# Optimization experiments

Measured on AMD Instinct MI355X. Metric: run time of the kernel, lower is better.

Reference implementation:

```python
import jax, jax.numpy as jnp
import numpy as np

N = 50000      # nodes
E = 800000     # edges per relation/layer
L = 2          # GCN layer_num
D = 128        # input_dim == output_dim


def setup_inputs() -> dict:
    key = jax.random.key(0)
    ks = jax.random.split(key, 11)
    x = jax.random.normal(ks[0], (N, D), jnp.float32)
    hidden = jax.random.normal(ks[1], (N, D), jnp.float32)
    adj_src = jax.random.randint(ks[2], (L, E), 0, N)
    adj_dst = jax.random.randint(ks[3], (L, E), 0, N)
    adj_w = jax.random.uniform(ks[4], (L, E), jnp.float32)
    std = 1.0 / np.sqrt(D)  # reset_parameters: uniform(-std, std)
    def u(k, shape):
        return jax.random.uniform(k, shape, jnp.float32, -std, std)
    gcn_W = u(ks[5], (L, D, D))
    gcn_b = u(ks[6], (L, D))
    x2h_W = u(ks[7], (D, 3 * D))
    x2h_b = u(ks[8], (3 * D,))
    h2h_W = u(ks[9], (D, 3 * D))
    h2h_b = u(ks[10], (3 * D,))
    return dict(x=x, hidden=hidden, adj_src=adj_src, adj_dst=adj_dst, adj_w=adj_w,
                gcn_W=gcn_W, gcn_b=gcn_b, x2h_W=x2h_W, x2h_b=x2h_b,
                h2h_W=h2h_W, h2h_b=h2h_b)


def reference(x, hidden, adj_src, adj_dst, adj_w, gcn_W, gcn_b,
              x2h_W, x2h_b, h2h_W, h2h_b):
    # MRGCN: layer_num GCN layers, layer l uses relation l's sparse adjacency.
    h = x
    for l in range(L):
        support = h @ gcn_W[l]                              # [N, D]
        msg = support[adj_src[l]] * adj_w[l][:, None]       # [E, D] irregular gather
        agg = jax.ops.segment_sum(msg, adj_dst[l], num_segments=N)  # spmm scatter-add
        h = jax.nn.relu(agg + gcn_b[l])
    # GRU gate chain (dropout=0 / eval mode)
    gate_x = h @ x2h_W + x2h_b                              # [N, 3D]
    gate_h = hidden @ h2h_W + h2h_b                         # [N, 3D]
    i_r, i_i, i_n = jnp.split(gate_x, 3, axis=1)
    h_r, h_i, h_n = jnp.split(gate_h, 3, axis=1)
    resetgate = jax.nn.sigmoid(i_r + h_r)
    inputgate = jax.nn.sigmoid(i_i + h_i)
    newgate = jnp.tanh(i_n + resetgate * h_n)
    hy = newgate + inputgate * (hidden - newgate)
    return hy
```

## Files before the change

kernel.cpp:

```cpp
#include <hip/hip_runtime.h>

#define D 128
#define RPW 8
#define ROWS_PB 32

typedef __attribute__((ext_vector_type(8))) short short8;
typedef __attribute__((ext_vector_type(4))) float f32x4;

static __device__ __forceinline__ ushort f2bf(float f) {
    unsigned u = __float_as_uint(f);
    unsigned r = (u + 0x7fffu + ((u >> 16) & 1u)) >> 16;
    return (ushort)r;
}

static __device__ __forceinline__ void gemm_body(float* sw, float (*sh)[D],
                                                 const float* __restrict__ in,
                                                 const float* __restrict__ W,
                                                 ushort* __restrict__ outb,
                                                 int N, int bid, int tid) {
    int row0 = bid * ROWS_PB;
    for (int j = tid; j < D * D / 4; j += 256)
        ((float4*)sw)[j] = ((const float4*)W)[j];
    for (int i = tid; i < ROWS_PB * (D / 4); i += 256) {
        int r = i >> 5, c4 = i & 31;
        int row = row0 + r;
        float4 v = (row < N) ? ((const float4*)(in + (size_t)row * D))[c4]
                             : make_float4(0.f, 0.f, 0.f, 0.f);
        ((float4*)sh)[i] = v;
    }
    __syncthreads();
    int wid = tid >> 6, lane = tid & 63;
    int rb = wid * RPW;
    float acc0[RPW], acc1[RPW];
#pragma unroll
    for (int r = 0; r < RPW; ++r) { acc0[r] = 0.f; acc1[r] = 0.f; }
    for (int k = 0; k < D; k += 4) {
        float w0[4], w1[4];
#pragma unroll
        for (int kk = 0; kk < 4; ++kk) {
            w0[kk] = sw[(k + kk) * D + lane];
            w1[kk] = sw[(k + kk) * D + lane + 64];
        }
#pragma unroll
        for (int r = 0; r < RPW; ++r) {
            float4 a4 = *(const float4*)&sh[rb + r][k];
            acc0[r] = fmaf(a4.x, w0[0], acc0[r]); acc1[r] = fmaf(a4.x, w1[0], acc1[r]);
            acc0[r] = fmaf(a4.y, w0[1], acc0[r]); acc1[r] = fmaf(a4.y, w1[1], acc1[r]);
            acc0[r] = fmaf(a4.z, w0[2], acc0[r]); acc1[r] = fmaf(a4.z, w1[2], acc1[r]);
            acc0[r] = fmaf(a4.w, w0[3], acc0[r]); acc1[r] = fmaf(a4.w, w1[3], acc1[r]);
        }
    }
#pragma unroll
    for (int r = 0; r < RPW; ++r) {
        int row = row0 + rb + r;
        if (row < N) {
            outb[(size_t)row * D + lane] = f2bf(acc0[r]);
            outb[(size_t)row * D + lane + 64] = f2bf(acc1[r]);
        }
    }
}

__global__ __launch_bounds__(256) void fused_sgc(const float* __restrict__ x,
                                                 const float* __restrict__ W0,
                                                 ushort* __restrict__ Abf, int N,
                                                 const int* __restrict__ adj_dst,
                                                 int* __restrict__ counts,
                                                 ushort* __restrict__ pl, int E2, int E,
                                                 const float* __restrict__ Wx,
                                                 const float* __restrict__ Wh,
                                                 ushort* __restrict__ wxt,
                                                 ushort* __restrict__ wht,
                                                 int GB, int SB) {
    __shared__ float sw[D * D];
    __shared__ float sh[ROWS_PB][D];
    int bid = blockIdx.x, tid = threadIdx.x;
    if (bid < GB) {
        gemm_body(sw, sh, x, W0, Abf, N, bid, tid);
    } else if (bid < GB + SB) {
        int i = (bid - GB) * 256 + tid;
        if (i < E2) {
            int off = (i >= E) ? N : 0;
            pl[i] = (ushort)atomicAdd(&counts[off + adj_dst[i]], 1);
        }
    } else {
        int i = (bid - GB - SB) * 256 + tid;
        if (i < 384 * 128) {
            int c = i >> 7, k = i & 127;
            wxt[i] = f2bf(Wx[(size_t)k * 384 + c]);
            wht[i] = f2bf(Wh[(size_t)k * 384 + c]);
        }
    }
}

__global__ __launch_bounds__(256) void gemm_rowbatch_bf(const float* __restrict__ in,
                                                        const float* __restrict__ W,
                                                        ushort* __restrict__ outb, int N) {
    __shared__ float sw[D * D];
    __shared__ float sh[ROWS_PB][D];
    gemm_body(sw, sh, in, W, outb, N, blockIdx.x, threadIdx.x);
}

__global__ void zero_int4(int4* __restrict__ p, int n4) {
    int i = blockIdx.x * blockDim.x + threadIdx.x;
    if (i < n4) p[i] = make_int4(0, 0, 0, 0);
}

__global__ __launch_bounds__(256) void scan_partial(const int4* __restrict__ counts4,
                                                    int* __restrict__ bsum) {
    int b = blockIdx.x, t = threadIdx.x;
    int4 c0 = counts4[(size_t)b * 512 + t * 2];
    int4 c1 = counts4[(size_t)b * 512 + t * 2 + 1];
    int s = c0.x + c0.y + c0.z + c0.w + c1.x + c1.y + c1.z + c1.w;
#pragma unroll
    for (int d = 1; d < 64; d <<= 1) s += __shfl_xor(s, d);
    __shared__ int ws[4];
    if ((t & 63) == 0) ws[t >> 6] = s;
    __syncthreads();
    if (t == 0) bsum[b] = ws[0] + ws[1] + ws[2] + ws[3];
}

__global__ void scan_base(const int* __restrict__ bsum, int* __restrict__ bbase, int nb) {
    int lane = threadIdx.x;
    int run = 0;
    for (int c = 0; c < nb; c += 64) {
        int v = (c + lane < nb) ? bsum[c + lane] : 0;
        int inc = v;
#pragma unroll
        for (int d = 1; d < 64; d <<= 1) {
            int y = __shfl_up(inc, d);
            if (lane >= d) inc += y;
        }
        if (c + lane < nb) bbase[c + lane] = run + inc - v;
        run += __shfl(inc, 63);
    }
}

__global__ __launch_bounds__(256) void scan_apply(const int4* __restrict__ counts4,
                                                  const int* __restrict__ bbase,
                                                  int4* __restrict__ off4) {
    __shared__ int ts[256];
    int b = blockIdx.x, t = threadIdx.x;
    int4 c0 = counts4[(size_t)b * 512 + t * 2];
    int4 c1 = counts4[(size_t)b * 512 + t * 2 + 1];
    int s = c0.x + c0.y + c0.z + c0.w + c1.x + c1.y + c1.z + c1.w;
    ts[t] = s;
    __syncthreads();
    for (int d = 1; d < 256; d <<= 1) {
        int x = ts[t];
        int y = (t >= d) ? ts[t - d] : 0;
        __syncthreads();
        ts[t] = x + y;
        __syncthreads();
    }
    int base = bbase[b] + ((t == 0) ? 0 : ts[t - 1]);
    int4 o0, o1;
    o0.x = base;
    o0.y = o0.x + c0.x;
    o0.z = o0.y + c0.y;
    o0.w = o0.z + c0.z;
    o1.x = o0.w + c0.w;
    o1.y = o1.x + c1.x;
    o1.z = o1.y + c1.y;
    o1.w = o1.z + c1.z;
    off4[(size_t)b * 512 + t * 2] = o0;
    off4[(size_t)b * 512 + t * 2 + 1] = o1;
}

__global__ void place2_kernel(const int* __restrict__ src, const int* __restrict__ dst,
                              const float* __restrict__ w,
                              const int* __restrict__ offsets2,
                              const ushort* __restrict__ pl,
                              int2* __restrict__ srcw0, int2* __restrict__ srcw1,
                              int E, int E2, int N) {
    int i = blockIdx.x * blockDim.x + threadIdx.x;
    if (i >= E2) return;
    int l1 = i >= E;
    int node = dst[i];
    int p = offsets2[(l1 ? N : 0) + node] - (l1 ? E : 0) + (int)pl[i];
    int2 v = make_int2(src[i], __float_as_int(w[i]));
    (l1 ? srcw1 : srcw0)[p] = v;
}

__global__ void gather_nodes(const ushort* __restrict__ supb, const int2* __restrict__ srcw,
                             const int* __restrict__ offsets, int sub,
                             const float* __restrict__ bias,
                             float* __restrict__ out, int N) {
    int node = (blockIdx.x * blockDim.x + threadIdx.x) >> 6;
    int lane = threadIdx.x & 63;
    if (node >= N) return;
    int lo = offsets[node] - sub, hi = offsets[node + 1] - sub;
    float ax = 0.f, ay = 0.f;
    int c = lane * 2;
    const ushort* base = supb + c;
    int j = lo;
    for (; j + 8 <= hi; j += 8) {
        int2 s[8];
        uint v[8];
#pragma unroll
        for (int u = 0; u < 8; ++u) s[u] = srcw[j + u];
#pragma unroll
        for (int u = 0; u < 8; ++u)
            v[u] = *(const uint*)(base + ((size_t)s[u].x << 7));
#pragma unroll
        for (int u = 0; u < 8; ++u) {
            float wt = __int_as_float(s[u].y);
            ax = fmaf(wt, __uint_as_float(v[u] << 16), ax);
            ay = fmaf(wt, __uint_as_float(v[u] & 0xffff0000u), ay);
        }
    }
    for (; j < hi; ++j) {
        int2 sw = srcw[j];
        float wt = __int_as_float(sw.y);
        uint v = *(const uint*)(base + ((size_t)sw.x << 7));
        ax = fmaf(wt, __uint_as_float(v << 16), ax);
        ay = fmaf(wt, __uint_as_float(v & 0xffff0000u), ay);
    }
    float2 bi = *(const float2*)(bias + c);
    float2 o;
    o.x = fmaxf(ax + bi.x, 0.f);
    o.y = fmaxf(ay + bi.y, 0.f);
    *(float2*)(out + (size_t)node * D + c) = o;
}

#define QROWS 192
#define KPAD 136
__global__ __launch_bounds__(256) void gru_mfma_lds(const float* __restrict__ h,
                                                    const float* __restrict__ hidden,
                                                    const ushort* __restrict__ wxt,
                                                    const ushort* __restrict__ wht,
                                                    const float* __restrict__ bx,
                                                    const float* __restrict__ bh,
                                                    float* __restrict__ out, int N) {
    __shared__ ushort lw[QROWS * KPAD];
    int tid = threadIdx.x;
    int wid = tid >> 6, lane = tid & 63;
    int nstripes = (N + 15) >> 4;
    int stripe = blockIdx.x * 4 + wid;
    bool live = stripe < nstripes;
    int row0 = stripe * 16;
    int lr = lane & 15;
    int lk = (lane >> 4) * 8;

    short8 Ah[4], Ad[4];
    if (live) {
        const float* hrow = h + (size_t)(row0 + lr) * D + lk;
        const float* drow = hidden + (size_t)(row0 + lr) * D + lk;
#pragma unroll
        for (int ks = 0; ks < 4; ++ks) {
            float4 a0 = *(const float4*)(hrow + ks * 32);
            float4 a1 = *(const float4*)(hrow + ks * 32 + 4);
            float4 c0 = *(const float4*)(drow + ks * 32);
            float4 c1 = *(const float4*)(drow + ks * 32 + 4);
            short8 va, vc;
            va[0] = f2bf(a0.x); va[1] = f2bf(a0.y); va[2] = f2bf(a0.z); va[3] = f2bf(a0.w);
            va[4] = f2bf(a1.x); va[5] = f2bf(a1.y); va[6] = f2bf(a1.z); va[7] = f2bf(a1.w);
            vc[0] = f2bf(c0.x); vc[1] = f2bf(c0.y); vc[2] = f2bf(c0.z); vc[3] = f2bf(c0.w);
            vc[4] = f2bf(c1.x); vc[5] = f2bf(c1.y); vc[6] = f2bf(c1.z); vc[7] = f2bf(c1.w);
            Ah[ks] = va;
            Ad[ks] = vc;
        }
    }
    int orow = row0 + (lane >> 4) * 4;

    for (int q = 0; q < 4; ++q) {
        if (q) __syncthreads();
        for (int j = tid; j < QROWS * 16; j += 256) {
            int chunk = j & 15;
            int row = j >> 4;
            int mat = row >= 96;
            int r = row - (mat ? 96 : 0);
            int g = r >> 5;
            int c = r & 31;
            const ushort* srcp = (mat ? wht : wxt)
                               + ((size_t)(g * 128 + q * 32 + c) << 7) + (chunk << 3);
            *(short8*)&lw[row * KPAD + chunk * 8] = *(const short8*)srcp;
        }
        __syncthreads();
        if (!live) continue;

#pragma unroll
        for (int mt = 0; mt < 2; ++mt) {
            int cl = mt * 16 + lr;
            const ushort* bx0 = lw + (0 * 32 + cl) * KPAD + lk;
            const ushort* bx1 = lw + (1 * 32 + cl) * KPAD + lk;
            const ushort* bx2 = lw + (2 * 32 + cl) * KPAD + lk;
            const ushort* bh0 = lw + ((96 + 0 * 32) + cl) * KPAD + lk;
            const ushort* bh1 = lw + ((96 + 1 * 32) + cl) * KPAD + lk;
            const ushort* bh2 = lw + ((96 + 2 * 32) + cl) * KPAD + lk;
            f32x4 ax0{}, ax1{}, ax2{}, ah0{}, ah1{}, ah2{};
#pragma unroll
            for (int ks = 0; ks < 4; ++ks) {
                short8 w0 = *(const short8*)(bx0 + ks * 32);
                short8 w1 = *(const short8*)(bx1 + ks * 32);
                short8 w2 = *(const short8*)(bx2 + ks * 32);
                short8 v0 = *(const short8*)(bh0 + ks * 32);
                short8 v1 = *(const short8*)(bh1 + ks * 32);
                short8 v2 = *(const short8*)(bh2 + ks * 32);
                ax0 = __builtin_amdgcn_mfma_f32_16x16x32_bf16(Ah[ks], w0, ax0, 0, 0, 0);
                ax1 = __builtin_amdgcn_mfma_f32_16x16x32_bf16(Ah[ks], w1, ax1, 0, 0, 0);
                ax2 = __builtin_amdgcn_mfma_f32_16x16x32_bf16(Ah[ks], w2, ax2, 0, 0, 0);
                ah0 = __builtin_amdgcn_mfma_f32_16x16x32_bf16(Ad[ks], v0, ah0, 0, 0, 0);
                ah1 = __builtin_amdgcn_mfma_f32_16x16x32_bf16(Ad[ks], v1, ah1, 0, 0, 0);
                ah2 = __builtin_amdgcn_mfma_f32_16x16x32_bf16(Ad[ks], v2, ah2, 0, 0, 0);
            }
            int col = q * 32 + mt * 16 + lr;
            float bxr = bx[col], bxi = bx[col + 128], bxn = bx[col + 256];
            float bhr = bh[col], bhi = bh[col + 128], bhn = bh[col + 256];
#pragma unroll
            for (int r = 0; r < 4; ++r) {
                int row = orow + r;
                if (row < N) {
                    float ir = ax0[r] + bxr, hr = ah0[r] + bhr;
                    float ii = ax1[r] + bxi, hi = ah1[r] + bhi;
                    float in_ = ax2[r] + bxn, hn = ah2[r] + bhn;
                    float rg = 1.f / (1.f + __expf(-(ir + hr)));
                    float ig = 1.f / (1.f + __expf(-(ii + hi)));
                    float nx = in_ + rg * hn;
                    float ng = 1.f - 2.f / (__expf(2.f * nx) + 1.f);
                    float hv = hidden[(size_t)row * D + col];
                    out[(size_t)row * D + col] = ng + ig * (hv - ng);
                }
            }
        }
    }
}

extern "C" void kernel_launch(void* const* d_in, const int* in_sizes, int n_in,
                              void* d_out, int out_size, void* d_ws, size_t ws_size,
                              hipStream_t stream) {
    const float* x      = (const float*)d_in[0];
    const float* hidden = (const float*)d_in[1];
    const int*   adj_src = (const int*)d_in[2];
    const int*   adj_dst = (const int*)d_in[3];
    const float* adj_w   = (const float*)d_in[4];
    const float* gcn_W   = (const float*)d_in[5];
    const float* gcn_b   = (const float*)d_in[6];
    const float* x2h_W   = (const float*)d_in[7];
    const float* x2h_b   = (const float*)d_in[8];
    const float* h2h_W   = (const float*)d_in[9];
    const float* h2h_b   = (const float*)d_in[10];
    float* out = (float*)d_out;

    const int L = 2;
    const int N = in_sizes[0] / D;
    const int E = in_sizes[2] / L;
    const size_t nd = (size_t)N * D;

    const int twoN   = 2 * N;
    const int NB     = (twoN + 2047) / 2048;
    const int padded = NB * 2048;

    char* ws = (char*)d_ws;
    ushort* Abf     = (ushort*)ws;                ws += nd * 2;
    float*  B       = (float*)ws;                 ws += nd * 4;
    int*   counts2  = (int*)ws;                   ws += (size_t)padded * 4;
    int*   offsets2 = (int*)ws;                   ws += ((size_t)padded + 64) * 4;
    int*   bsum     = (int*)ws;                   ws += ((size_t)NB + 64) * 4;
    int*   bbase    = (int*)ws;                   ws += ((size_t)NB + 64) * 4;
    int2*  srcw0    = (int2*)ws;                  ws += (size_t)E * 8;
    int2*  srcw1    = (int2*)ws;                  ws += (size_t)E * 8;
    ushort* pl      = (ushort*)ws;                ws += (size_t)2 * E * 2;
    ushort* wxt     = (ushort*)ws;                ws += (size_t)384 * 128 * 2;
    ushort* wht     = (ushort*)ws;                ws += (size_t)384 * 128 * 2;

    dim3 blk(256);
    int batch_blocks = (N + ROWS_PB - 1) / ROWS_PB;
    int gat_blocks   = (N + 3) / 4;
    int e2_blocks    = (2 * E + 255) / 256;
    int zero_blocks  = (padded / 4 + 255) / 256;
    int convw_blocks = (384 * 128 + 255) / 256;
    int nstripes     = (N + 15) / 16;
    int gru_blocks   = (nstripes + 3) / 4;

    zero_int4<<<zero_blocks, blk, 0, stream>>>((int4*)counts2, padded / 4);
    fused_sgc<<<batch_blocks + e2_blocks + convw_blocks, blk, 0, stream>>>(
        x, gcn_W, Abf, N, adj_dst, counts2, pl, 2 * E, E,
        x2h_W, h2h_W, wxt, wht, batch_blocks, e2_blocks);
    scan_partial<<<NB, blk, 0, stream>>>((const int4*)counts2, bsum);
    scan_base<<<1, 64, 0, stream>>>(bsum, bbase, NB);
    scan_apply<<<NB, blk, 0, stream>>>((const int4*)counts2, bbase, (int4*)offsets2);
    place2_kernel<<<e2_blocks, blk, 0, stream>>>(adj_src, adj_dst, adj_w, offsets2, pl,
                                                 srcw0, srcw1, E, 2 * E, N);
    gather_nodes<<<gat_blocks, blk, 0, stream>>>(Abf, srcw0, offsets2, 0,
                                                 gcn_b, B, N);
    gemm_rowbatch_bf<<<batch_blocks, blk, 0, stream>>>(B, gcn_W + (size_t)D * D, Abf, N);
    gather_nodes<<<gat_blocks, blk, 0, stream>>>(Abf, srcw1, offsets2 + N, E,
                                                 gcn_b + D, B, N);
    gru_mfma_lds<<<gru_blocks, blk, 0, stream>>>(B, hidden, wxt, wht, x2h_b, h2h_b, out, N);
}
```

Baseline: 327.3 us.

## Fuse layer-0 gather with layer-1 GEMM and store intermediates in bf16

Layer 0's gather/aggregate is fused with the layer-1 dense GEMM in one kernel. Each wave gathers a row, applies bias and ReLU, then multiplies it by W1 held in LDS, which removes the fp32 intermediate round trip and a kernel launch. The second gather now writes bf16 output, which the GRU kernel loads directly without converting. The first fused kernel also interleaves GEMM blocks with count-atomic blocks in a 1:4 pattern. The fused kernel loads the full 64KB W1 into LDS for every 16-node block, which adds LDS traffic and lowers occupancy, and the per-row GEMM runs serially inside each wave.

```diff
diff --git a/kernel.cpp b/kernel.cpp
--- a/kernel.cpp
+++ b/kernel.cpp
@@ -65,39 +65,35 @@
                                                  ushort* __restrict__ Abf, int N,
                                                  const int* __restrict__ adj_dst,
                                                  int* __restrict__ counts,
-                                                 ushort* __restrict__ pl, int E2, int E,
+                                                 ushort* __restrict__ pl, int E2,
+                                                 int E, int GB,
                                                  const float* __restrict__ Wx,
                                                  const float* __restrict__ Wh,
                                                  ushort* __restrict__ wxt,
-                                                 ushort* __restrict__ wht,
-                                                 int GB, int SB) {
+                                                 ushort* __restrict__ wht) {
     __shared__ float sw[D * D];
     __shared__ float sh[ROWS_PB][D];
     int bid = blockIdx.x, tid = threadIdx.x;
-    if (bid < GB) {
-        gemm_body(sw, sh, x, W0, Abf, N, bid, tid);
-    } else if (bid < GB + SB) {
-        int i = (bid - GB) * 256 + tid;
-        if (i < E2) {
-            int off = (i >= E) ? N : 0;
-            pl[i] = (ushort)atomicAdd(&counts[off + adj_dst[i]], 1);
+    int five = GB * 5;
+    if (bid < five) {
+        int g = bid / 5, j = bid - g * 5;
+        if (j == 0) {
+            gemm_body(sw, sh, x, W0, Abf, N, g, tid);
+        } else {
+            int i = (g * 4 + j - 1) * 256 + tid;
+            if (i < E2) {
+                int off = (i >= E) ? N : 0;
+                pl[i] = (ushort)atomicAdd(&counts[off + adj_dst[i]], 1);
+            }
         }
     } else {
-        int i = (bid - GB - SB) * 256 + tid;
+        int i = (bid - five) * 256 + tid;
         if (i < 384 * 128) {
             int c = i >> 7, k = i & 127;
             wxt[i] = f2bf(Wx[(size_t)k * 384 + c]);
             wht[i] = f2bf(Wh[(size_t)k * 384 + c]);
         }
     }
-}
-
-__global__ __launch_bounds__(256) void gemm_rowbatch_bf(const float* __restrict__ in,
-                                                        const float* __restrict__ W,
-                                                        ushort* __restrict__ outb, int N) {
-    __shared__ float sw[D * D];
-    __shared__ float sh[ROWS_PB][D];
-    gemm_body(sw, sh, in, W, outb, N, blockIdx.x, threadIdx.x);
 }
 
 __global__ void zero_int4(int4* __restrict__ p, int n4) {
@@ -181,17 +177,11 @@
     (l1 ? srcw1 : srcw0)[p] = v;
 }
 
-__global__ void gather_nodes(const ushort* __restrict__ supb, const int2* __restrict__ srcw,
-                             const int* __restrict__ offsets, int sub,
-                             const float* __restrict__ bias,
-                             float* __restrict__ out, int N) {
-    int node = (blockIdx.x * blockDim.x + threadIdx.x) >> 6;
-    int lane = threadIdx.x & 63;
-    if (node >= N) return;
-    int lo = offsets[node] - sub, hi = offsets[node + 1] - sub;
-    float ax = 0.f, ay = 0.f;
-    int c = lane * 2;
-    const ushort* base = supb + c;
+static __device__ __forceinline__ void gather_row(const ushort* __restrict__ base,
+                                                  const int2* __restrict__ srcw,
+                                                  int lo, int hi,
+                                                  float& ax, float& ay) {
+    ax = 0.f; ay = 0.f;
     int j = lo;
     for (; j + 8 <= hi; j += 8) {
         int2 s[8];
@@ -215,16 +205,70 @@
         ax = fmaf(wt, __uint_as_float(v << 16), ax);
         ay = fmaf(wt, __uint_as_float(v & 0xffff0000u), ay);
     }
+}
+
+__global__ __launch_bounds__(256) void gather_gemm(const ushort* __restrict__ supb,
+                                                   const int2* __restrict__ srcw,
+                                                   const int* __restrict__ offsets,
+                                                   const float* __restrict__ bias,
+                                                   const float* __restrict__ W1,
+                                                   ushort* __restrict__ outb, int N) {
+    __shared__ float sw1[D * D];
+    __shared__ float rowbuf[4][D];
+    int tid = threadIdx.x;
+    for (int j = tid; j < D * D / 4; j += 256)
+        ((float4*)sw1)[j] = ((const float4*)W1)[j];
+    __syncthreads();
+    int wid = tid >> 6, lane = tid & 63;
+    int c = lane * 2;
+    const ushort* base = supb + c;
+#pragma unroll
+    for (int r = 0; r < 4; ++r) {
+        int node = blockIdx.x * 16 + wid * 4 + r;
+        if (node >= N) break;
+        int lo = offsets[node], hi = offsets[node + 1];
+        float ax, ay;
+        gather_row(base, srcw, lo, hi, ax, ay);
+        float2 bi = *(const float2*)(bias + c);
+        rowbuf[wid][c] = fmaxf(ax + bi.x, 0.f);
+        rowbuf[wid][c + 1] = fmaxf(ay + bi.y, 0.f);
+        float acc0 = 0.f, acc1 = 0.f;
+        for (int k = 0; k < D; k += 4) {
+            float4 rv = *(const float4*)&rowbuf[wid][k];
+            acc0 = fmaf(rv.x, sw1[(k + 0) * D + lane], acc0);
+            acc1 = fmaf(rv.x, sw1[(k + 0) * D + lane + 64], acc1);
+            acc0 = fmaf(rv.y, sw1[(k + 1) * D + lane], acc0);
+            acc1 = fmaf(rv.y, sw1[(k + 1) * D + lane + 64], acc1);
+            acc0 = fmaf(rv.z, sw1[(k + 2) * D + lane], acc0);
+            acc1 = fmaf(rv.z, sw1[(k + 2) * D + lane + 64], acc1);
+            acc0 = fmaf(rv.w, sw1[(k + 3) * D + lane], acc0);
+            acc1 = fmaf(rv.w, sw1[(k + 3) * D + lane + 64], acc1);
+        }
+        outb[(size_t)node * D + lane] = f2bf(acc0);
+        outb[(size_t)node * D + lane + 64] = f2bf(acc1);
+    }
+}
+
+__global__ void gather_nodes_bf(const ushort* __restrict__ supb,
+                                const int2* __restrict__ srcw,
+                                const int* __restrict__ offsets, int sub,
+                                const float* __restrict__ bias,
+                                ushort* __restrict__ outb, int N) {
+    int node = (blockIdx.x * blockDim.x + threadIdx.x) >> 6;
+    int lane = threadIdx.x & 63;
+    if (node >= N) return;
+    int lo = offsets[node] - sub, hi = offsets[node + 1] - sub;
+    int c = lane * 2;
+    float ax, ay;
+    gather_row(supb + c, srcw, lo, hi, ax, ay);
     float2 bi = *(const float2*)(bias + c);
-    float2 o;
-    o.x = fmaxf(ax + bi.x, 0.f);
-    o.y = fmaxf(ay + bi.y, 0.f);
-    *(float2*)(out + (size_t)node * D + c) = o;
+    uint pk = ((uint)f2bf(fmaxf(ay + bi.y, 0.f)) << 16) | (uint)f2bf(fmaxf(ax + bi.x, 0.f));
+    *(uint*)(outb + (size_t)node * D + c) = pk;
 }
 
 #define QROWS 192
 #define KPAD 136
-__global__ __launch_bounds__(256) void gru_mfma_lds(const float* __restrict__ h,
+__global__ __launch_bounds__(256) void gru_mfma_lds(const ushort* __restrict__ hb,
                                                     const float* __restrict__ hidden,
                                                     const ushort* __restrict__ wxt,
                                                     const ushort* __restrict__ wht,
@@ -243,20 +287,16 @@
 
     short8 Ah[4], Ad[4];
     if (live) {
-        const float* hrow = h + (size_t)(row0 + lr) * D + lk;
+        const ushort* hrow = hb + (size_t)(row0 + lr) * D + lk;
         const float* drow = hidden + (size_t)(row0 + lr) * D + lk;
 #pragma unroll
         for (int ks = 0; ks < 4; ++ks) {
-            float4 a0 = *(const float4*)(hrow + ks * 32);
-            float4 a1 = *(const float4*)(hrow + ks * 32 + 4);
+            Ah[ks] = *(const short8*)(hrow + ks * 32);
             float4 c0 = *(const float4*)(drow + ks * 32);
             float4 c1 = *(const float4*)(drow + ks * 32 + 4);
-            short8 va, vc;
-            va[0] = f2bf(a0.x); va[1] = f2bf(a0.y); va[2] = f2bf(a0.z); va[3] = f2bf(a0.w);
-            va[4] = f2bf(a1.x); va[5] = f2bf(a1.y); va[6] = f2bf(a1.z); va[7] = f2bf(a1.w);
+            short8 vc;
             vc[0] = f2bf(c0.x); vc[1] = f2bf(c0.y); vc[2] = f2bf(c0.z); vc[3] = f2bf(c0.w);
             vc[4] = f2bf(c1.x); vc[5] = f2bf(c1.y); vc[6] = f2bf(c1.z); vc[7] = f2bf(c1.w);
-            Ah[ks] = va;
             Ad[ks] = vc;
         }
     }
@@ -352,7 +392,8 @@
 
     char* ws = (char*)d_ws;
     ushort* Abf     = (ushort*)ws;                ws += nd * 2;
-    float*  B       = (float*)ws;                 ws += nd * 4;
+    ushort* Abf2    = (ushort*)ws;                ws += nd * 2;
+    ushort* Bbf     = (ushort*)ws;                ws += nd * 2;
     int*   counts2  = (int*)ws;                   ws += (size_t)padded * 4;
     int*   offsets2 = (int*)ws;                   ws += ((size_t)padded + 64) * 4;
     int*   bsum     = (int*)ws;                   ws += ((size_t)NB + 64) * 4;
@@ -369,22 +410,23 @@
     int e2_blocks    = (2 * E + 255) / 256;
     int zero_blocks  = (padded / 4 + 255) / 256;
     int convw_blocks = (384 * 128 + 255) / 256;
+    int gg_blocks    = (N + 15) / 16;
     int nstripes     = (N + 15) / 16;
     int gru_blocks   = (nstripes + 3) / 4;
 
     zero_int4<<<zero_blocks, blk, 0, stream>>>((int4*)counts2, padded / 4);
-    fused_sgc<<<batch_blocks + e2_blocks + convw_blocks, blk, 0, stream>>>(
-        x, gcn_W, Abf, N, adj_dst, counts2, pl, 2 * E, E,
-        x2h_W, h2h_W, wxt, wht, batch_blocks, e2_blocks);
+    fused_sgc<<<batch_blocks * 5 + convw_blocks, blk, 0, stream>>>(
+        x, gcn_W, Abf, N, adj_dst, counts2, pl, 2 * E, E, batch_blocks,
+        x2h_W, h2h_W, wxt, wht);
     scan_partial<<<NB, blk, 0, stream>>>((const int4*)counts2, bsum);
     scan_base<<<1, 64, 0, stream>>>(bsum, bbase, NB);
     scan_apply<<<NB, blk, 0, stream>>>((const int4*)counts2, bbase, (int4*)offsets2);
     place2_kernel<<<e2_blocks, blk, 0, stream>>>(adj_src, adj_dst, adj_w, offsets2, pl,
                                                  srcw0, srcw1, E, 2 * E, N);
-    gather_nodes<<<gat_blocks, blk, 0, stream>>>(Abf, srcw0, offsets2, 0,
-                                                 gcn_b, B, N);
-    gemm_rowbatch_bf<<<batch_blocks, blk, 0, stream>>>(B, gcn_W + (size_t)D * D, Abf, N);
-    gather_nodes<<<gat_blocks, blk, 0, stream>>>(Abf, srcw1, offsets2 + N, E,
-                                                 gcn_b + D, B, N);
-    gru_mfma_lds<<<gru_blocks, blk, 0, stream>>>(B, hidden, wxt, wht, x2h_b, h2h_b, out, N);
-}
+    gather_gemm<<<gg_blocks, blk, 0, stream>>>(Abf, srcw0, offsets2, gcn_b,
+                                               gcn_W + (size_t)D * D, Abf2, N);
+    gather_nodes_bf<<<gat_blocks, blk, 0, stream>>>(Abf2, srcw1, offsets2 + N, E,
+                                                    gcn_b + D, Bbf, N);
+    gru_mfma_lds<<<gru_blocks, blk, 0, stream>>>(Bbf, hidden, wxt, wht, x2h_b, h2h_b,
+                                                 out, N);
+}
```

Result: slower. 373.4 us (+14.1%).
